# Kernel tuning notes

Measured on AMD Instinct MI355X. Metric: run time of the kernel, lower is better.

## Reference

```python
import math
import jax, jax.numpy as jnp
import numpy as np

DIM = 1024
FFN_DIM = 4096
NUM_HEADS = 16
HEAD_DIM = DIM // NUM_HEADS
SCALE = 1.0 / math.sqrt(HEAD_DIM)
EPS = 1e-5


def _layer_norm(x, gamma, beta):
    mu = jnp.mean(x, axis=-1, keepdims=True)
    var = jnp.mean(jnp.square(x - mu), axis=-1, keepdims=True)
    return (x - mu) * jax.lax.rsqrt(var + EPS) * gamma + beta


def _gelu_erf(x):
    # matches torch GELU module: x * 0.5 * (1 + erf(x / sqrt(2)))
    return x * 0.5 * (1.0 + jax.lax.erf(x / math.sqrt(2.0)))


def setup_inputs() -> dict:
    key = jax.random.key(0)
    ks = jax.random.split(key, 12)
    B, L = 2, 2048
    s = 0.02
    inp = {
        "x": jax.random.normal(ks[0], (B, L, DIM), dtype=jnp.float32),
        "g1": jnp.ones((DIM,), jnp.float32),
        "b1": jnp.zeros((DIM,), jnp.float32),
        "Wq": jax.random.normal(ks[1], (DIM, DIM), jnp.float32) * s,
        "bq": jnp.zeros((DIM,), jnp.float32),
        "Wk": jax.random.normal(ks[2], (DIM, DIM), jnp.float32) * s,
        "bk": jnp.zeros((DIM,), jnp.float32),
        "Wv": jax.random.normal(ks[3], (DIM, DIM), jnp.float32) * s,
        "bv": jnp.zeros((DIM,), jnp.float32),
        "Wo": jax.random.normal(ks[4], (DIM, DIM), jnp.float32) * s,
        "bo": jnp.zeros((DIM,), jnp.float32),
        "g2": jnp.ones((DIM,), jnp.float32),
        "b2": jnp.zeros((DIM,), jnp.float32),
        "W1": jax.random.normal(ks[5], (FFN_DIM, DIM), jnp.float32) * s,
        "bf1": jnp.zeros((FFN_DIM,), jnp.float32),
        "W2": jax.random.normal(ks[6], (DIM, FFN_DIM), jnp.float32) * s,
        "bf2": jnp.zeros((DIM,), jnp.float32),
    }
    return inp


def reference(x, g1, b1, Wq, bq, Wk, bk, Wv, bv, Wo, bo, g2, b2, W1, bf1, W2, bf2):
    B, L, C = x.shape
    n, c = NUM_HEADS, HEAD_DIM

    # ---- pre-norm self-attention ----
    h = _layer_norm(x, g1, b1)
    q = (h @ Wq.T + bq).reshape(B, L, n, c)
    k = (h @ Wk.T + bk).reshape(B, L, n, c)
    v = (h @ Wv.T + bv).reshape(B, L, n, c)
    attn = SCALE * jnp.einsum('binc,bjnc->bnij', q, k)   # [B, n, L, L]
    attn = jax.nn.softmax(attn, axis=-1)
    o = jnp.einsum('bnij,bjnc->binc', attn, v).reshape(B, L, C)
    x = x + (o @ Wo.T + bo)

    # ---- pre-norm FFN (GELU, erf form) ----
    h = _layer_norm(x, g2, b2)
    h = _gelu_erf(h @ W1.T + bf1)
    x = x + (h @ W2.T + bf2)
    return x
```

## Files before the change

kernel.cpp:

```cpp
#include <hip/hip_runtime.h>
#include <hip/hip_bf16.h>
#include <math.h>

typedef unsigned short u16;
typedef __attribute__((ext_vector_type(8))) __bf16 bf16x8;
typedef __attribute__((ext_vector_type(4))) float f32x4;

#define DIM   1024
#define LSEQ  2048
#define BTOK  4096
#define HD    64
#define FFN   4096
#define QSCL  0.18033688011112042f

#if __has_builtin(__builtin_amdgcn_exp2f)
#define EXP2(x) __builtin_amdgcn_exp2f(x)
#else
#define EXP2(x) exp2f(x)
#endif

__device__ __forceinline__ u16 f2bf(float f) {
  unsigned u = __builtin_bit_cast(unsigned, f);
  u += 0x7FFFu + ((u >> 16) & 1u);
  return (u16)(u >> 16);
}
__device__ __forceinline__ unsigned pk2(float a, float b) {
  return (unsigned)f2bf(a) | ((unsigned)f2bf(b) << 16);
}
__device__ __forceinline__ unsigned cvtpk(float lo, float hi) {
  unsigned r;
  asm("v_cvt_pk_bf16_f32 %0, %1, %2" : "=v"(r) : "v"(lo), "v"(hi));
  return r;
}
__device__ __forceinline__ f32x4 mfma16(bf16x8 a, bf16x8 b, f32x4 c) {
  return __builtin_amdgcn_mfma_f32_16x16x32_bf16(a, b, c, 0, 0, 0);
}
__device__ __forceinline__ void gload16(const void* g, void* l) {
  __builtin_amdgcn_global_load_lds((const __attribute__((address_space(1))) char*)g,
                                   (__attribute__((address_space(3))) char*)l, 16, 0, 0);
}
__device__ __forceinline__ float gelu_t(float v) {
  float v3 = v * v * v;
  float tt = fmaf(-0.10296766f, v3, -2.30258509f * v);
  return v * __builtin_amdgcn_rcpf(1.0f + EXP2(tt));
}

__global__ __launch_bounds__(256) void ln_kernel(const float* __restrict__ x,
                                                 const float* __restrict__ g,
                                                 const float* __restrict__ bta,
                                                 u16* __restrict__ out) {
  int row = blockIdx.x, t = threadIdx.x;
  const float* xr = x + (size_t)row * DIM;
  float4 xv = *(const float4*)(xr + t * 4);
  float s  = xv.x + xv.y + xv.z + xv.w;
  float ss = xv.x * xv.x + xv.y * xv.y + xv.z * xv.z + xv.w * xv.w;
#pragma unroll
  for (int m = 32; m >= 1; m >>= 1) {
    s  += __shfl_xor(s, m);
    ss += __shfl_xor(ss, m);
  }
  __shared__ float red[8];
  if ((t & 63) == 0) { red[(t >> 6) * 2] = s; red[(t >> 6) * 2 + 1] = ss; }
  __syncthreads();
  s  = red[0] + red[2] + red[4] + red[6];
  ss = red[1] + red[3] + red[5] + red[7];
  float mu  = s * (1.0f / DIM);
  float var = ss * (1.0f / DIM) - mu * mu;
  float rs  = rsqrtf(var + 1e-5f);
  float4 gv = *(const float4*)(g + t * 4);
  float4 bv = *(const float4*)(bta + t * 4);
  uint2 o;
  o.x = pk2((xv.x - mu) * rs * gv.x + bv.x, (xv.y - mu) * rs * gv.y + bv.y);
  o.y = pk2((xv.z - mu) * rs * gv.z + bv.z, (xv.w - mu) * rs * gv.w + bv.w);
  *(uint2*)(out + (size_t)row * DIM + t * 4) = o;
}

__global__ __launch_bounds__(256) void wcvt4(const float* __restrict__ Wq, const float* __restrict__ Wk,
                                             const float* __restrict__ Wv, const float* __restrict__ Wo,
                                             u16* __restrict__ dst) {
  int b = blockIdx.x;
  int r = b >> 9;
  const float* s = (r == 0) ? Wq : (r == 1) ? Wk : (r == 2) ? Wv : Wo;
  size_t i = (((size_t)(b & 511)) * 256 + threadIdx.x) * 8;
  float4 f0 = *(const float4*)(s + i), f1 = *(const float4*)(s + i + 4);
  uint4 o = { pk2(f0.x, f0.y), pk2(f0.z, f0.w), pk2(f1.x, f1.y), pk2(f1.z, f1.w) };
  *(uint4*)(dst + ((size_t)r << 20) + i) = o;
}
__global__ __launch_bounds__(256) void wcvt2(const float* __restrict__ W1, const float* __restrict__ W2,
                                             u16* __restrict__ d1, u16* __restrict__ d2) {
  int b = blockIdx.x;
  const float* s = (b < 2048) ? W1 : W2;
  u16* d = (b < 2048) ? d1 : d2;
  size_t i = (((size_t)(b & 2047)) * 256 + threadIdx.x) * 8;
  float4 f0 = *(const float4*)(s + i), f1 = *(const float4*)(s + i + 4);
  uint4 o = { pk2(f0.x, f0.y), pk2(f0.z, f0.w), pk2(f1.x, f1.y), pk2(f1.z, f1.w) };
  *(uint4*)(d + i) = o;
}

__global__ __launch_bounds__(256) void transpose_v(const u16* __restrict__ v,
                                                   u16* __restrict__ vt) {
  __shared__ u16 tls[64][80];
  int jb = blockIdx.x, bh = blockIdx.y, b = bh >> 4, h = bh & 15;
  int t = threadIdx.x;
  int r = t >> 2, seg = t & 3;
  const u16* src = v + (size_t)(b * LSEQ + jb * 64 + r) * DIM + h * HD + seg * 16;
  *(uint4*)&tls[r][seg * 16]     = *(const uint4*)src;
  *(uint4*)&tls[r][seg * 16 + 8] = *(const uint4*)(src + 8);
  __syncthreads();
  int c = t >> 2, jseg = t & 3;
  u16 tmp[16] __attribute__((aligned(16)));
#pragma unroll
  for (int i = 0; i < 16; i++) tmp[i] = tls[jseg * 16 + i][c];
  u16* dst = vt + ((size_t)bh * HD + c) * LSEQ + jb * 64 + jseg * 16;
  *(uint4*)dst       = *(const uint4*)tmp;
  *(uint4*)(dst + 8) = *(const uint4*)(tmp + 8);
}

struct GArg { const u16* Wb; const float* bias; u16* outB; float oscale; };

template <int EPI, int BM, int DEPTH>
__global__ __launch_bounds__(256) void gemm4(const u16* __restrict__ A,
                                             GArg g0, GArg g1, GArg g2,
                                             const float* __restrict__ resid,
                                             float* __restrict__ outF,
                                             int N, int K, int nbPerW) {
  constexpr int WM  = BM / 32;
  constexpr int LPT = BM / 64 + 2;
  constexpr int ABUF = BM * 64;
  constexpr int BBUF = 8192;
  constexpr int VX  = (DEPTH - 2) * LPT;
  __shared__ u16 lsa[DEPTH][BM * 32];
  __shared__ u16 lsb[DEPTH][128 * 32];
  const int t = threadIdx.x;
  const int w = t >> 6, l = t & 63, l15 = l & 15, lg = l >> 4;
  const int wr = w >> 1, wc = w & 1;
  const int nwg = gridDim.x * gridDim.y;
  int flat = blockIdx.y * gridDim.x + blockIdx.x;
  flat = (flat & 7) * (nwg >> 3) + (flat >> 3);
  const int bx = flat % gridDim.x, by = flat / gridDim.x;
  const int sel = bx / nbPerW, nb = bx % nbPerW;
  GArg G = (sel == 0) ? g0 : ((sel == 1) ? g1 : g2);
  const int n0 = nb * 128, m0 = by * BM;

  f32x4 acc[WM][4];
#pragma unroll
  for (int m = 0; m < WM; m++)
#pragma unroll
    for (int n = 0; n < 4; n++) acc[m][n] = (f32x4){0.f, 0.f, 0.f, 0.f};

  const int grow = t >> 2;
  const int gcol = 8 * ((t & 3) ^ ((t >> 3) & 3));
  const u16* Asrc = A + (size_t)(m0 + grow) * K + gcol;
  const u16* Bsrc = G.Wb + (size_t)(n0 + grow) * K + gcol;
  const int rs = (l15 >> 1) & 3;

  const char* aadr = (const char*)lsa + (wr * (BM / 2) + l15) * 64 + (lg ^ rs) * 16;
  const char* badr = (const char*)lsb + (wc * 64 + l15) * 64 + (lg ^ rs) * 16;

  auto stage = [&](int k0, int buf) {
#pragma unroll
    for (int i = 0; i < BM / 64; i++)
      gload16(Asrc + (size_t)i * 64 * K + k0, (char*)lsa + buf * ABUF + i * 4096 + w * 1024);
#pragma unroll
    for (int i = 0; i < 2; i++)
      gload16(Bsrc + (size_t)i * 64 * K + k0, (char*)lsb + buf * BBUF + i * 4096 + w * 1024);
  };

#pragma unroll
  for (int p = 0; p < DEPTH - 1; p++) stage(p << 5, p);

  const int NT = K >> 5;
  int bufR = 0, bufW = DEPTH - 1;
  for (int it = 0; it < NT; it++) {
    if constexpr (VX == 4) asm volatile("s_waitcnt vmcnt(4)" ::: "memory");
    else if constexpr (VX == 6) asm volatile("s_waitcnt vmcnt(6)" ::: "memory");
    else asm volatile("s_waitcnt vmcnt(0)" ::: "memory");
    __builtin_amdgcn_s_barrier();
    if (it + DEPTH - 1 < NT) stage((it + DEPTH - 1) << 5, bufW);

    const char* ap = aadr + bufR * ABUF;
    const char* bp = badr + bufR * BBUF;
    bf16x8 af[WM], bfr[4];
#pragma unroll
    for (int m = 0; m < WM; m++)
      af[m] = *(const bf16x8*)(ap + m * 1024);
#pragma unroll
    for (int n = 0; n < 4; n++)
      bfr[n] = *(const bf16x8*)(bp + n * 1024);
    __builtin_amdgcn_s_setprio(1);
#pragma unroll
    for (int m = 0; m < WM; m++)
#pragma unroll
      for (int n = 0; n < 4; n++)
        acc[m][n] = mfma16(af[m], bfr[n], acc[m][n]);
    __builtin_amdgcn_s_setprio(0);
    bufR = (bufR + 1 == DEPTH) ? 0 : bufR + 1;
    bufW = (bufW + 1 == DEPTH) ? 0 : bufW + 1;
  }

#pragma unroll
  for (int m = 0; m < WM; m++) {
    const int row = m0 + wr * (BM / 2) + m * 16 + lg * 4;
#pragma unroll
    for (int n = 0; n < 4; n++) {
      const int col = n0 + wc * 64 + n * 16 + l15;
      const float bias = G.bias[col];
#pragma unroll
      for (int r = 0; r < 4; r++) {
        const float v = acc[m][n][r] + bias;
        const size_t idx = (size_t)(row + r) * N + col;
        if (EPI == 0)      G.outB[idx] = f2bf(v * G.oscale);
        else if (EPI == 1) outF[idx] = v + resid[idx];
        else               G.outB[idx] = f2bf(gelu_t(v));
      }
    }
  }
}

__global__ __launch_bounds__(256, 4) void attn5(const u16* __restrict__ q,
                                                const u16* __restrict__ k,
                                                const u16* __restrict__ vt,
                                                u16* __restrict__ o) {
  __shared__ __align__(16) char smem[40960];
  const int t = threadIdx.x, w = t >> 6, l = t & 63, l15 = l & 15, lg = l >> 4;
  int flat = blockIdx.y * gridDim.x + blockIdx.x;
  flat = (flat & 7) * 128 + (flat >> 3);
  const int qbk = flat & 31, bh = flat >> 5;
  const int b = bh >> 4, h = bh & 15;
  const int qrow0 = b * LSEQ + qbk * 64 + w * 16;
  const int r7 = l15 & 7;
  const int c0 = lg ^ r7;

  bf16x8 av[2];
#pragma unroll
  for (int i = 0; i < 2; i++)
    av[i] = *(const bf16x8*)(q + (size_t)(qrow0 + l15) * DIM + h * HD + i * 32 + lg * 8);

  const char* adrA  = smem + l15 * 128 + c0 * 16;
  const char* adrB  = smem + l15 * 128 + (c0 ^ 4) * 16;
  const char* padrA = smem + 32768 + w * 2048 + l15 * 128 + c0 * 16;
  const char* padrB = smem + 32768 + w * 2048 + l15 * 128 + (c0 ^ 4) * 16;
  char* pwa[4];
#pragma unroll
  for (int cb = 0; cb < 4; cb++)
    pwa[cb] = smem + 32768 + w * 2048 + l15 * 128 +
              (((2 * cb + (lg >> 1)) ^ r7) * 16) + (lg & 1) * 8;

  const int grow = t >> 3, gchk = t & 7;
  const u16* ksrc = k + (size_t)(b * LSEQ + grow) * DIM + h * HD + 8 * (gchk ^ (grow & 7));
  const u16* vsrc = vt + ((size_t)bh * HD + grow) * LSEQ + 8 * (gchk ^ (grow & 7));

  f32x4 oacc[4];
#pragma unroll
  for (int cb = 0; cb < 4; cb++) oacc[cb] = (f32x4){0.f, 0.f, 0.f, 0.f};
  f32x4 minit = (f32x4){0.f, 0.f, 0.f, 0.f};
  float lsum = 0.f;

  auto issueTile = [&](int jt, int buf) {
    const u16* kp = ksrc + (size_t)jt * DIM;
    const u16* vp = vsrc + jt;
#pragma unroll
    for (int i = 0; i < 2; i++) {
      gload16(kp + (size_t)i * 32 * DIM,  smem + buf * 8192 + i * 4096 + w * 1024);
      gload16(vp + (size_t)i * 32 * LSEQ, smem + 16384 + buf * 8192 + i * 4096 + w * 1024);
    }
  };

  issueTile(0, 0);
  for (int it = 0; it < LSEQ / 64; it++) {
    const int buf = it & 1;
    __syncthreads();
    if (it + 1 < LSEQ / 64) issueTile((it + 1) * 64, buf ^ 1);
    const int ko = buf * 8192;

    f32x4 s[4];
    const char* kA = adrA + ko;
    const char* kB = adrB + ko;
    __builtin_amdgcn_s_setprio(1);
#pragma unroll
    for (int cb = 0; cb < 4; cb++) {
      bf16x8 kf0 = *(const bf16x8*)(kA + cb * 2048);
      bf16x8 kf1 = *(const bf16x8*)(kB + cb * 2048);
      s[cb] = mfma16(kf0, av[0], minit);
      s[cb] = mfma16(kf1, av[1], s[cb]);
    }
    __builtin_amdgcn_s_setprio(0);

    float tm = fmaxf(fmaxf(fmaxf(s[0][0], s[0][1]), fmaxf(s[0][2], s[0][3])),
                     fmaxf(fmaxf(fmaxf(s[1][0], s[1][1]), fmaxf(s[1][2], s[1][3])),
                           fmaxf(fmaxf(fmaxf(s[2][0], s[2][1]), fmaxf(s[2][2], s[2][3])),
                                 fmaxf(fmaxf(s[3][0], s[3][1]), fmaxf(s[3][2], s[3][3])))));
    if (__any(tm > 8.0f)) {
      float tr = fmaxf(tm, __shfl_xor(tm, 16));
      tr = fmaxf(tr, __shfl_xor(tr, 32));
      const float d = fmaxf(tr, 0.f);
      const float scl = EXP2(-d);
      const f32x4 dv = (f32x4){d, d, d, d};
      lsum *= scl;
      minit -= dv;
#pragma unroll
      for (int cb = 0; cb < 4; cb++) s[cb] -= dv;
#pragma unroll
      for (int r = 0; r < 4; r++) {
        const float so = __shfl(scl, lg * 4 + r);
#pragma unroll
        for (int cb = 0; cb < 4; cb++) oacc[cb][r] *= so;
      }
    }
    float ps = 0.f;
    uint2 pk[4];
#pragma unroll
    for (int cb = 0; cb < 4; cb++) {
      float a0 = EXP2(s[cb][0]);
      float a1 = EXP2(s[cb][1]);
      float a2 = EXP2(s[cb][2]);
      float a3 = EXP2(s[cb][3]);
      ps += (a0 + a1) + (a2 + a3);
      pk[cb].x = cvtpk(a0, a1);
      pk[cb].y = cvtpk(a2, a3);
    }
    lsum += ps;
#pragma unroll
    for (int cb = 0; cb < 4; cb++) *(uint2*)pwa[cb] = pk[cb];

    const char* vA = adrA + ko + 16384;
    const char* vB = adrB + ko + 16384;
    bf16x8 pa0 = *(const bf16x8*)padrA;
    bf16x8 pa1 = *(const bf16x8*)padrB;
    __builtin_amdgcn_s_setprio(1);
#pragma unroll
    for (int cb = 0; cb < 4; cb++) {
      bf16x8 vf0 = *(const bf16x8*)(vA + cb * 2048);
      oacc[cb] = mfma16(pa0, vf0, oacc[cb]);
    }
#pragma unroll
    for (int cb = 0; cb < 4; cb++) {
      bf16x8 vf1 = *(const bf16x8*)(vB + cb * 2048);
      oacc[cb] = mfma16(pa1, vf1, oacc[cb]);
    }
    __builtin_amdgcn_s_setprio(0);
  }

  float rl = lsum + __shfl_xor(lsum, 16);
  rl += __shfl_xor(rl, 32);
#pragma unroll
  for (int r = 0; r < 4; r++) {
    const float lo = __shfl(rl, lg * 4 + r);
    const float rcp = 1.0f / lo;
#pragma unroll
    for (int cb = 0; cb < 4; cb++) {
      o[(size_t)(qrow0 + lg * 4 + r) * DIM + h * HD + cb * 16 + l15] =
          f2bf(oacc[cb][r] * rcp);
    }
  }
}

extern "C" void kernel_launch(void* const* d_in, const int* in_sizes, int n_in,
                              void* d_out, int out_size, void* d_ws, size_t ws_size,
                              hipStream_t stream) {
  const float* x   = (const float*)d_in[0];
  const float* g1  = (const float*)d_in[1];
  const float* b1  = (const float*)d_in[2];
  const float* Wq  = (const float*)d_in[3];
  const float* bq  = (const float*)d_in[4];
  const float* Wk  = (const float*)d_in[5];
  const float* bk  = (const float*)d_in[6];
  const float* Wv  = (const float*)d_in[7];
  const float* bv  = (const float*)d_in[8];
  const float* Wo  = (const float*)d_in[9];
  const float* bo  = (const float*)d_in[10];
  const float* g2  = (const float*)d_in[11];
  const float* b2  = (const float*)d_in[12];
  const float* W1  = (const float*)d_in[13];
  const float* bf1 = (const float*)d_in[14];
  const float* W2  = (const float*)d_in[15];
  const float* bf2 = (const float*)d_in[16];
  float* out = (float*)d_out;

  const size_t E = (size_t)BTOK * DIM;
  u16* h     = (u16*)d_ws;
  u16* qb    = h + E;
  u16* kbuf  = qb + E;
  u16* vbuf  = kbuf + E;
  u16* vtb   = vbuf + E;
  u16* wqkvo = vtb + E;
  u16* ob    = vbuf;
  u16* W1b   = qb;
  u16* W2b   = kbuf;
  u16* mid   = vbuf;
  u16* h2    = h;
  float* x2  = out;

  u16* Wqb = wqkvo;
  u16* Wkb = wqkvo + ((size_t)1 << 20);
  u16* Wvb = wqkvo + ((size_t)2 << 20);
  u16* Wob = wqkvo + ((size_t)3 << 20);

  wcvt4<<<dim3(2048), dim3(256), 0, stream>>>(Wq, Wk, Wv, Wo, wqkvo);
  ln_kernel<<<dim3(BTOK), dim3(256), 0, stream>>>(x, g1, b1, h);
  gemm4<0, 128, 3><<<dim3(24, BTOK / 128), 256, 0, stream>>>(
      h, GArg{Wqb, bq, qb, QSCL}, GArg{Wkb, bk, kbuf, 1.0f}, GArg{Wvb, bv, vbuf, 1.0f},
      nullptr, nullptr, DIM, DIM, 8);
  transpose_v<<<dim3(32, 32), 256, 0, stream>>>(vbuf, vtb);
  attn5<<<dim3(LSEQ / 64, 32), 256, 0, stream>>>(qb, kbuf, vtb, ob);
  {
    GArg s{Wob, bo, nullptr, 1.0f};
    gemm4<1, 64, 4><<<dim3(8, BTOK / 64), 256, 0, stream>>>(ob, s, s, s, x, x2, DIM, DIM, 8);
  }
  wcvt2<<<dim3(4096), dim3(256), 0, stream>>>(W1, W2, W1b, W2b);
  ln_kernel<<<dim3(BTOK), dim3(256), 0, stream>>>(x2, g2, b2, h2);
  {
    GArg s{W1b, bf1, mid, 1.0f};
    gemm4<2, 128, 3><<<dim3(32, BTOK / 128), 256, 0, stream>>>(h2, s, s, s, nullptr, nullptr, FFN, DIM, 32);
  }
  {
    GArg s{W2b, bf2, nullptr, 1.0f};
    gemm4<1, 64, 4><<<dim3(8, BTOK / 64), 256, 0, stream>>>(mid, s, s, s, x2, out, DIM, FFN, 8);
  }
}
```

Before: 258.7 us.

## Split-K the N=1024 GEMMs with atomic accumulation and residual prefill

The output-projection and FFN-down GEMMs now split K across two blocks (grid z=2) and accumulate with float atomicAdd into the output buffer. A new prefill kernel seeds that buffer with residual plus bias for the Wo projection. The FFN-down GEMM adds its bias only in the z=0 slice, on top of the residual already in the buffer. Pipeline depth drops from 4 to 3 and the wait count is tightened on the last iteration. The goal is to double the block count for these narrow GEMMs, at the cost of an extra pass, atomic traffic and non-deterministic summation order.

```diff
diff --git a/kernel.cpp b/kernel.cpp
--- a/kernel.cpp
+++ b/kernel.cpp
@@ -116,14 +116,23 @@
   *(uint4*)(dst + 8) = *(const uint4*)(tmp + 8);
 }
 
+__global__ __launch_bounds__(256) void prefill(float* __restrict__ io,
+                                               const float* __restrict__ a,
+                                               const float* __restrict__ bias) {
+  size_t i = ((size_t)blockIdx.x * 256 + threadIdx.x) * 4;
+  float4 va = *(const float4*)(a + i);
+  float4 vc = *(const float4*)(bias + (i & (DIM - 1)));
+  va.x += vc.x; va.y += vc.y; va.z += vc.z; va.w += vc.w;
+  *(float4*)(io + i) = va;
+}
+
 struct GArg { const u16* Wb; const float* bias; u16* outB; float oscale; };
 
 template <int EPI, int BM, int DEPTH>
 __global__ __launch_bounds__(256) void gemm4(const u16* __restrict__ A,
                                              GArg g0, GArg g1, GArg g2,
-                                             const float* __restrict__ resid,
                                              float* __restrict__ outF,
-                                             int N, int K, int nbPerW) {
+                                             int N, int Kstride, int Kiter, int nbPerW) {
   constexpr int WM  = BM / 32;
   constexpr int LPT = BM / 64 + 2;
   constexpr int ABUF = BM * 64;
@@ -141,6 +150,8 @@
   const int sel = bx / nbPerW, nb = bx % nbPerW;
   GArg G = (sel == 0) ? g0 : ((sel == 1) ? g1 : g2);
   const int n0 = nb * 128, m0 = by * BM;
+  const int z = blockIdx.z;
+  const int koff = z * Kiter;
 
   f32x4 acc[WM][4];
 #pragma unroll
@@ -150,8 +161,8 @@
 
   const int grow = t >> 2;
   const int gcol = 8 * ((t & 3) ^ ((t >> 3) & 3));
-  const u16* Asrc = A + (size_t)(m0 + grow) * K + gcol;
-  const u16* Bsrc = G.Wb + (size_t)(n0 + grow) * K + gcol;
+  const u16* Asrc = A + (size_t)(m0 + grow) * Kstride + koff + gcol;
+  const u16* Bsrc = G.Wb + (size_t)(n0 + grow) * Kstride + koff + gcol;
   const int rs = (l15 >> 1) & 3;
 
   const char* aadr = (const char*)lsa + (wr * (BM / 2) + l15) * 64 + (lg ^ rs) * 16;
@@ -160,22 +171,29 @@
   auto stage = [&](int k0, int buf) {
 #pragma unroll
     for (int i = 0; i < BM / 64; i++)
-      gload16(Asrc + (size_t)i * 64 * K + k0, (char*)lsa + buf * ABUF + i * 4096 + w * 1024);
+      gload16(Asrc + (size_t)i * 64 * Kstride + k0, (char*)lsa + buf * ABUF + i * 4096 + w * 1024);
 #pragma unroll
     for (int i = 0; i < 2; i++)
-      gload16(Bsrc + (size_t)i * 64 * K + k0, (char*)lsb + buf * BBUF + i * 4096 + w * 1024);
+      gload16(Bsrc + (size_t)i * 64 * Kstride + k0, (char*)lsb + buf * BBUF + i * 4096 + w * 1024);
   };
 
 #pragma unroll
   for (int p = 0; p < DEPTH - 1; p++) stage(p << 5, p);
 
-  const int NT = K >> 5;
+  const int NT = Kiter >> 5;
   int bufR = 0, bufW = DEPTH - 1;
   for (int it = 0; it < NT; it++) {
-    if constexpr (VX == 4) asm volatile("s_waitcnt vmcnt(4)" ::: "memory");
-    else if constexpr (VX == 6) asm volatile("s_waitcnt vmcnt(6)" ::: "memory");
-    else asm volatile("s_waitcnt vmcnt(0)" ::: "memory");
+    if (it + 1 < NT) {
+      if constexpr (VX == 3)      asm volatile("s_waitcnt vmcnt(3)" ::: "memory");
+      else if constexpr (VX == 4) asm volatile("s_waitcnt vmcnt(4)" ::: "memory");
+      else if constexpr (VX == 6) asm volatile("s_waitcnt vmcnt(6)" ::: "memory");
+      else                        asm volatile("s_waitcnt vmcnt(0)" ::: "memory");
+    } else {
+      asm volatile("s_waitcnt vmcnt(0)" ::: "memory");
+    }
     __builtin_amdgcn_s_barrier();
+    asm volatile("" ::: "memory");
+
     if (it + DEPTH - 1 < NT) stage((it + DEPTH - 1) << 5, bufW);
 
     const char* ap = aadr + bufR * ABUF;
@@ -204,13 +222,15 @@
 #pragma unroll
     for (int n = 0; n < 4; n++) {
       const int col = n0 + wc * 64 + n * 16 + l15;
-      const float bias = G.bias[col];
+      float bcol;
+      if (EPI == 4) bcol = (z == 0 && G.bias != nullptr) ? G.bias[col] : 0.f;
+      else          bcol = G.bias[col];
 #pragma unroll
       for (int r = 0; r < 4; r++) {
-        const float v = acc[m][n][r] + bias;
+        const float v = acc[m][n][r] + bcol;
         const size_t idx = (size_t)(row + r) * N + col;
         if (EPI == 0)      G.outB[idx] = f2bf(v * G.oscale);
-        else if (EPI == 1) outF[idx] = v + resid[idx];
+        else if (EPI == 4) atomicAdd(&outF[idx], v);
         else               G.outB[idx] = f2bf(gelu_t(v));
       }
     }
@@ -400,21 +420,25 @@
   ln_kernel<<<dim3(BTOK), dim3(256), 0, stream>>>(x, g1, b1, h);
   gemm4<0, 128, 3><<<dim3(24, BTOK / 128), 256, 0, stream>>>(
       h, GArg{Wqb, bq, qb, QSCL}, GArg{Wkb, bk, kbuf, 1.0f}, GArg{Wvb, bv, vbuf, 1.0f},
-      nullptr, nullptr, DIM, DIM, 8);
+      nullptr, DIM, DIM, DIM, 8);
   transpose_v<<<dim3(32, 32), 256, 0, stream>>>(vbuf, vtb);
   attn5<<<dim3(LSEQ / 64, 32), 256, 0, stream>>>(qb, kbuf, vtb, ob);
+  prefill<<<dim3(4096), dim3(256), 0, stream>>>(out, x, bo);
   {
-    GArg s{Wob, bo, nullptr, 1.0f};
-    gemm4<1, 64, 4><<<dim3(8, BTOK / 64), 256, 0, stream>>>(ob, s, s, s, x, x2, DIM, DIM, 8);
+    GArg s{Wob, nullptr, nullptr, 1.0f};
+    gemm4<4, 64, 3><<<dim3(8, BTOK / 64, 2), 256, 0, stream>>>(
+        ob, s, s, s, out, DIM, DIM, 512, 8);
   }
   wcvt2<<<dim3(4096), dim3(256), 0, stream>>>(W1, W2, W1b, W2b);
   ln_kernel<<<dim3(BTOK), dim3(256), 0, stream>>>(x2, g2, b2, h2);
   {
     GArg s{W1b, bf1, mid, 1.0f};
-    gemm4<2, 128, 3><<<dim3(32, BTOK / 128), 256, 0, stream>>>(h2, s, s, s, nullptr, nullptr, FFN, DIM, 32);
+    gemm4<2, 128, 3><<<dim3(32, BTOK / 128), 256, 0, stream>>>(
+        h2, s, s, s, nullptr, FFN, DIM, DIM, 32);
   }
   {
     GArg s{W2b, bf2, nullptr, 1.0f};
-    gemm4<1, 64, 4><<<dim3(8, BTOK / 64), 256, 0, stream>>>(mid, s, s, s, x2, out, DIM, FFN, 8);
-  }
-}
+    gemm4<4, 64, 3><<<dim3(8, BTOK / 64, 2), 256, 0, stream>>>(
+        mid, s, s, s, out, DIM, FFN, 2048, 8);
+  }
+}
```

Result: slower. 286.3 us (+10.6%).
